# Kernel optimization log

Measured on AMD Instinct MI355X. Metric: run time of the kernel, lower is better.

## Reference

```python
import jax, jax.numpy as jnp
import numpy as np

D_MODEL = 1024
NUM_HEAD = 16
D_HEAD = D_MODEL // NUM_HEAD


def setup_inputs() -> dict:
    key = jax.random.key(0)
    kx, kq, kk, kv, ko = jax.random.split(key, 5)
    x = jax.random.normal(kx, (2, 2048, D_MODEL), dtype=jnp.float32)
    p_q = jax.random.normal(kq, (D_MODEL, D_MODEL), dtype=jnp.float32)
    p_k = jax.random.normal(kk, (D_MODEL, D_MODEL), dtype=jnp.float32)
    p_v = jax.random.normal(kv, (D_MODEL, D_MODEL), dtype=jnp.float32)
    p_o = jax.random.normal(ko, (D_MODEL, D_MODEL), dtype=jnp.float32)
    return {"x": x, "p_q": p_q, "p_k": p_k, "p_v": p_v, "p_o": p_o}


def reference(x, p_q, p_k, p_v, p_o):
    B, S, _ = x.shape
    # project: weight viewed as [H, d_head, d_model]; out[b,h,s,d] = sum_m x[b,s,m] W[h,d,m]
    wq = p_q.reshape(NUM_HEAD, D_HEAD, D_MODEL)
    wk = p_k.reshape(NUM_HEAD, D_HEAD, D_MODEL)
    wv = p_v.reshape(NUM_HEAD, D_HEAD, D_MODEL)
    q = jnp.einsum('bsm,hdm->bhsd', x, wq)
    k = jnp.einsum('bsm,hdm->bhsd', x, wk)
    v = jnp.einsum('bsm,hdm->bhsd', x, wv)
    # full causal attention, scores scaled by 1/sqrt(d_head)
    scores = jnp.einsum('bhqd,bhkd->bhqk', q, k) / jnp.sqrt(jnp.float32(D_HEAD))
    causal = jnp.tril(jnp.ones((S, S), dtype=bool))
    scores = jnp.where(causal, scores, -jnp.inf)
    attn = jax.nn.softmax(scores, axis=-1)
    out = jnp.einsum('bhqk,bhkd->bhqd', attn, v)
    out = out.transpose(0, 2, 1, 3).reshape(B, S, D_MODEL)  # [B,S,H*d_head]
    # output proj: einsum '... d1, d2 d1 -> ... d2' == out @ p_o.T
    return jnp.einsum('bsm,nm->bsn', out, p_o)
```

## Files before the change

### kernel.cpp

```cpp
#include <hip/hip_runtime.h>
#include <stdint.h>

#define D_MODEL 1024
#define SEQ     2048
#define NHEAD   16
#define BATCH   2
#define NROWS   (BATCH*SEQ)

typedef _Float16 f16;
typedef _Float16 f16x8 __attribute__((ext_vector_type(8)));
typedef _Float16 f16x4 __attribute__((ext_vector_type(4)));
typedef __fp16   h16x2 __attribute__((ext_vector_type(2)));
typedef float    f32x4 __attribute__((ext_vector_type(4)));

#define MFMA16 __builtin_amdgcn_mfma_f32_16x16x32_f16

__device__ __forceinline__ void gload16(const void* g, void* l) {
  __builtin_amdgcn_global_load_lds(
      (const __attribute__((address_space(1))) void*)g,
      (__attribute__((address_space(3))) void*)l, 16, 0, 0);
}

__device__ __forceinline__ int pkh2(float a, float b) {
  union { h16x2 h; int i; } u;
  u.h = __builtin_amdgcn_cvt_pkrtz(a, b);
  return u.i;
}

__global__ void split4_kernel(const float* __restrict__ in, f16* __restrict__ hi,
                              f16* __restrict__ lo, int n4, float scale) {
  int i = blockIdx.x * blockDim.x + threadIdx.x;
  if (i >= n4) return;
  float4 v = reinterpret_cast<const float4*>(in)[i];
  v.x *= scale; v.y *= scale; v.z *= scale; v.w *= scale;
  f16x4 h, l4;
  h[0] = (f16)v.x; h[1] = (f16)v.y; h[2] = (f16)v.z; h[3] = (f16)v.w;
  l4[0] = (f16)(v.x - (float)h[0]);
  l4[1] = (f16)(v.y - (float)h[1]);
  l4[2] = (f16)(v.z - (float)h[2]);
  l4[3] = (f16)(v.w - (float)h[3]);
  *reinterpret_cast<f16x4*>(hi + 4*(size_t)i) = h;
  *reinterpret_cast<f16x4*>(lo + 4*(size_t)i) = l4;
}

__global__ void prep_w_kernel(const float* __restrict__ pq, const float* __restrict__ pk,
                              const float* __restrict__ pv, const float* __restrict__ po,
                              f16* __restrict__ wq_hi, f16* __restrict__ wq_lo,
                              f16* __restrict__ wk_hi, f16* __restrict__ wk_lo,
                              f16* __restrict__ wv_h,  f16* __restrict__ wo_h,
                              int n4, float qscale) {
  int i = blockIdx.x * blockDim.x + threadIdx.x;
  if (i >= n4) return;
  {
    float4 v = reinterpret_cast<const float4*>(pq)[i];
    v.x *= qscale; v.y *= qscale; v.z *= qscale; v.w *= qscale;
    f16x4 h, l4;
    h[0] = (f16)v.x; h[1] = (f16)v.y; h[2] = (f16)v.z; h[3] = (f16)v.w;
    l4[0] = (f16)(v.x - (float)h[0]); l4[1] = (f16)(v.y - (float)h[1]);
    l4[2] = (f16)(v.z - (float)h[2]); l4[3] = (f16)(v.w - (float)h[3]);
    *reinterpret_cast<f16x4*>(wq_hi + 4*(size_t)i) = h;
    *reinterpret_cast<f16x4*>(wq_lo + 4*(size_t)i) = l4;
  }
  {
    float4 v = reinterpret_cast<const float4*>(pk)[i];
    f16x4 h, l4;
    h[0] = (f16)v.x; h[1] = (f16)v.y; h[2] = (f16)v.z; h[3] = (f16)v.w;
    l4[0] = (f16)(v.x - (float)h[0]); l4[1] = (f16)(v.y - (float)h[1]);
    l4[2] = (f16)(v.z - (float)h[2]); l4[3] = (f16)(v.w - (float)h[3]);
    *reinterpret_cast<f16x4*>(wk_hi + 4*(size_t)i) = h;
    *reinterpret_cast<f16x4*>(wk_lo + 4*(size_t)i) = l4;
  }
  {
    float4 v = reinterpret_cast<const float4*>(pv)[i];
    f16x4 h;
    h[0] = (f16)v.x; h[1] = (f16)v.y; h[2] = (f16)v.z; h[3] = (f16)v.w;
    *reinterpret_cast<f16x4*>(wv_h + 4*(size_t)i) = h;
  }
  {
    float4 v = reinterpret_cast<const float4*>(po)[i];
    f16x4 h;
    h[0] = (f16)v.x; h[1] = (f16)v.y; h[2] = (f16)v.z; h[3] = (f16)v.w;
    *reinterpret_cast<f16x4*>(wo_h + 4*(size_t)i) = h;
  }
}

template<bool F32_OUT, bool COLCHUNK>
__global__ __launch_bounds__(256, 2)
void gemm_nt(const f16* __restrict__ Ahi,
             const f16* __restrict__ Bhi,
             f16* __restrict__ Chi, float* __restrict__ Cf,
             int M, int N, int K)
{
  constexpr int B_OFF  = 8192;
  constexpr int STRIDE = 12288;
  __shared__ __align__(16) char smem[2 * STRIDE];

  const int tid = threadIdx.x;
  const int w = tid >> 6, l = tid & 63;
  const int wr = (w >> 1) * 64;
  const int wc = (w & 1) * 32;

  const int gx = gridDim.x, gy = gridDim.y;
  const int nwg = gx * gy;
  const int flat = blockIdx.y * gx + blockIdx.x;
  const int swz = (flat & 7) * (nwg >> 3) + (flat >> 3);
  const int bxn = COLCHUNK ? (swz / gy) : (swz % gx);
  const int byn = COLCHUNK ? (swz % gy) : (swz / gx);
  const int bm = byn * 128, bn = bxn * 64;

  f32x4 acc[4][2] = {};

  const int srow = tid >> 2;
  const int schunk = 8 * (((tid & 3) ^ ((srow >> 1) & 3)));

  auto stage = [&](int kt) {
    char* dst = smem + (kt & 1) * STRIDE;
    const int k0 = kt * 32;
    const f16* ga = Ahi + (size_t)(bm + srow) * K + k0 + schunk;
    gload16(ga,        dst + (w << 10));
    gload16(ga + 64*K, dst + 4096 + (w << 10));
    const f16* gb = Bhi + (size_t)(bn + srow) * K + k0 + schunk;
    gload16(gb,        dst + B_OFF + (w << 10));
  };

  const int nkt = K >> 5;
  stage(0);

  for (int kt = 0; kt < nkt; kt++) {
    if (kt + 1 < nkt) {
      stage(kt + 1);
      asm volatile("s_waitcnt vmcnt(3)" ::: "memory");
    } else {
      asm volatile("s_waitcnt vmcnt(0)" ::: "memory");
    }
    __builtin_amdgcn_s_barrier();

    const char* buf = smem + (kt & 1) * STRIDE;
    const int ar = (l & 15);
    const int ak = 16 * ((l >> 4) ^ ((ar >> 1) & 3));
    f16x8 a_hi[4];
#pragma unroll
    for (int mi = 0; mi < 4; mi++)
      a_hi[mi] = *(const f16x8*)(buf + (size_t)(wr + mi*16 + ar) * 64 + ak);
    __builtin_amdgcn_s_setprio(1);
#pragma unroll
    for (int ni = 0; ni < 2; ni++) {
      f16x8 b_hi = *(const f16x8*)(buf + B_OFF + (size_t)(wc + ni*16 + ar) * 64 + ak);
#pragma unroll
      for (int mi = 0; mi < 4; mi++)
        acc[mi][ni] = MFMA16(a_hi[mi], b_hi, acc[mi][ni], 0, 0, 0);
    }
    __builtin_amdgcn_s_setprio(0);
    __builtin_amdgcn_s_barrier();
  }

  const int crow0 = bm + wr + (l >> 4) * 4;
  const int ccol0 = bn + wc + (l & 15);
#pragma unroll
  for (int mi = 0; mi < 4; mi++) {
#pragma unroll
    for (int ni = 0; ni < 2; ni++) {
#pragma unroll
      for (int j = 0; j < 4; j++) {
        size_t idx = (size_t)(crow0 + mi*16 + j) * N + (ccol0 + ni*16);
        float v = acc[mi][ni][j];
        if (F32_OUT) Cf[idx] = v;
        else         Chi[idx] = (f16)v;
      }
    }
  }
}

__global__ __launch_bounds__(256, 2)
void gemm_qk(const f16* __restrict__ Ahi, const f16* __restrict__ Alo,
             const f16* __restrict__ Bqh, const f16* __restrict__ Bql,
             const f16* __restrict__ Bkh, const f16* __restrict__ Bkl,
             f16* __restrict__ Qh, f16* __restrict__ Qlo2,
             f16* __restrict__ Kh, f16* __restrict__ Klo2)
{
  constexpr int N = D_MODEL, K = D_MODEL;
  constexpr int STRIDE = 32768;
  __shared__ __align__(16) char smem[2 * STRIDE];

  const int tid = threadIdx.x;
  const int w = tid >> 6, l = tid & 63;
  const int wr = (w >> 1) * 64;
  const int wc = (w & 1) * 32;

  const int flat = blockIdx.y * 16 + blockIdx.x;
  const int swz = (flat & 7) * 64 + (flat >> 3);
  const int bm = (swz / 16) * 128, bn = (swz % 16) * 64;

  f32x4 accQ[4][2] = {}, accK[4][2] = {};

  const int srow = tid >> 2;
  const int schunk = 8 * (((tid & 3) ^ ((srow >> 1) & 3)));

  auto stage = [&](int kt) {
    char* dst = smem + (kt & 1) * STRIDE;
    const int k0 = kt * 32;
    const f16* ga = Ahi + (size_t)(bm + srow) * K + k0 + schunk;
    gload16(ga,        dst + (w << 10));
    gload16(ga + 64*K, dst + 4096 + (w << 10));
    const f16* gal = Alo + (size_t)(bm + srow) * K + k0 + schunk;
    gload16(gal,        dst + 8192 + (w << 10));
    gload16(gal + 64*K, dst + 12288 + (w << 10));
    const size_t bo = (size_t)(bn + srow) * K + k0 + schunk;
    gload16(Bqh + bo, dst + 16384 + (w << 10));
    gload16(Bql + bo, dst + 20480 + (w << 10));
    gload16(Bkh + bo, dst + 24576 + (w << 10));
    gload16(Bkl + bo, dst + 28672 + (w << 10));
  };

  const int nkt = K >> 5;
  stage(0);

  for (int kt = 0; kt < nkt; kt++) {
    if (kt + 1 < nkt) {
      stage(kt + 1);
      asm volatile("s_waitcnt vmcnt(8)" ::: "memory");
    } else {
      asm volatile("s_waitcnt vmcnt(0)" ::: "memory");
    }
    __builtin_amdgcn_s_barrier();

    const char* buf = smem + (kt & 1) * STRIDE;
    const int ar = (l & 15);
    const int ak = 16 * ((l >> 4) ^ ((ar >> 1) & 3));
    f16x8 a_hi[4], a_lo[4];
#pragma unroll
    for (int mi = 0; mi < 4; mi++) {
      a_hi[mi] = *(const f16x8*)(buf + (size_t)(wr + mi*16 + ar) * 64 + ak);
      a_lo[mi] = *(const f16x8*)(buf + 8192 + (size_t)(wr + mi*16 + ar) * 64 + ak);
    }
    __builtin_amdgcn_s_setprio(1);
#pragma unroll
    for (int ni = 0; ni < 2; ni++) {
      const int bo = (wc + ni*16 + ar) * 64 + ak;
      f16x8 bqh = *(const f16x8*)(buf + 16384 + bo);
      f16x8 bql = *(const f16x8*)(buf + 20480 + bo);
      f16x8 bkh = *(const f16x8*)(buf + 24576 + bo);
      f16x8 bkl = *(const f16x8*)(buf + 28672 + bo);
#pragma unroll
      for (int mi = 0; mi < 4; mi++) {
        accQ[mi][ni] = MFMA16(a_hi[mi], bqh, accQ[mi][ni], 0, 0, 0);
        accQ[mi][ni] = MFMA16(a_hi[mi], bql, accQ[mi][ni], 0, 0, 0);
        accQ[mi][ni] = MFMA16(a_lo[mi], bqh, accQ[mi][ni], 0, 0, 0);
        accK[mi][ni] = MFMA16(a_hi[mi], bkh, accK[mi][ni], 0, 0, 0);
        accK[mi][ni] = MFMA16(a_hi[mi], bkl, accK[mi][ni], 0, 0, 0);
        accK[mi][ni] = MFMA16(a_lo[mi], bkh, accK[mi][ni], 0, 0, 0);
      }
    }
    __builtin_amdgcn_s_setprio(0);
    __builtin_amdgcn_s_barrier();
  }

  const int crow0 = bm + wr + (l >> 4) * 4;
  const int ccol0 = bn + wc + (l & 15);
#pragma unroll
  for (int mi = 0; mi < 4; mi++) {
#pragma unroll
    for (int ni = 0; ni < 2; ni++) {
#pragma unroll
      for (int j = 0; j < 4; j++) {
        size_t idx = (size_t)(crow0 + mi*16 + j) * N + (ccol0 + ni*16);
        float qv = accQ[mi][ni][j];
        f16 qh = (f16)qv;
        Qh[idx] = qh;  Qlo2[idx] = (f16)(qv - (float)qh);
        float kv = accK[mi][ni][j];
        f16 kh = (f16)kv;
        Kh[idx] = kh;  Klo2[idx] = (f16)(kv - (float)kh);
      }
    }
  }
}

__global__ __launch_bounds__(512, 4)
void attn_kernel(const f16* __restrict__ Qhi, const f16* __restrict__ Qlo,
                 const f16* __restrict__ Khi, const f16* __restrict__ Klo,
                 const f16* __restrict__ VT, f16* __restrict__ Out)
{
  __shared__ __align__(16) char smem[49152];

  const int tid = threadIdx.x, w = tid >> 6, l = tid & 63;
  const int g = l >> 4, q4 = l & 15;
  const int wi = w & 3, grp = w >> 2;
  const int flat = blockIdx.x;
  const int xcd = flat & 7, slot = flat >> 3;
  const int bh = xcd * 4 + (slot >> 4);
  const int c = slot & 15;
  const int b = bh >> 4, h = bh & 15;
  const int bS = b * SEQ;
  const size_t hoff = (size_t)h * 64;
  const int T  = 64 - 2 * c;
  const int P1 = 2 * c + 2;
  const int P2 = 31 - 2 * c;

  int qw = (grp ? (31 - c) : c) * 64 + wi * 16;

  f16x8 qh[2], ql[2];
  auto loadQ = [&]() {
#pragma unroll
    for (int ks = 0; ks < 2; ks++) {
      const size_t base = (size_t)(bS + qw + q4) * D_MODEL + hoff + ks * 32 + g * 8;
      qh[ks] = *(const f16x8*)(Qhi + base);
      ql[ks] = *(const f16x8*)(Qlo + base);
    }
  };
  loadQ();

  f32x4 o[4] = {};
  float m_run = -INFINITY, l_run = 0.f;

  const int k_src = 8 * ((l & 7) ^ (l >> 3));
  const int v_src = 8 * ((l & 3) ^ ((l >> 2) & 3));

  auto stage = [&](int t) {
    const int kv0 = t * 32;
    char* sb = smem + (t & 3) * 12288;
    if (w < 4) {
      const f16* src = (w < 2) ? Khi : Klo;
      char* dstc = sb + ((w < 2) ? 0 : 4096);
      const int wi2 = w & 1;
#pragma unroll
      for (int gi = 0; gi < 2; gi++) {
        const int sub = 2 * wi2 + gi;
        const int row = 8 * sub + (l >> 3);
        gload16(src + (size_t)(bS + kv0 + row) * D_MODEL + hoff + k_src,
                dstc + sub * 1024);
      }
    } else if (w < 6) {
      const int wi2 = w - 4;
#pragma unroll
      for (int gi = 0; gi < 2; gi++) {
        const int sub = 2 * wi2 + gi;
        const int drow = 16 * sub + (l >> 2);
        gload16(VT + (hoff + drow) * (size_t)NROWS + bS + kv0 + v_src,
                sb + 8192 + sub * 1024);
      }
    }
  };

  const int idx_lo = (q4 + 32 * (g & 1)) * 4;
  const int idx_hi = idx_lo + 64;
  const bool upper = (l >= 32);

  auto compute = [&](int t) {
    const char* sb = smem + (t & 3) * 12288;
    const int kv0 = t * 32;

    f32x4 s[2] = {};
    __builtin_amdgcn_s_setprio(1);
#pragma unroll
    for (int ni = 0; ni < 2; ni++) {
      const int row = ni * 16 + q4;
#pragma unroll
      for (int ks = 0; ks < 2; ks++) {
        const int boff = row * 128 + 16 * ((ks * 4 + g) ^ (row & 7));
        f16x8 kh8 = *(const f16x8*)(sb + boff);
        f16x8 kl8 = *(const f16x8*)(sb + 4096 + boff);
        s[ni] = MFMA16(kh8, qh[ks], s[ni], 0, 0, 0);
        s[ni] = MFMA16(kh8, ql[ks], s[ni], 0, 0, 0);
        s[ni] = MFMA16(kl8, qh[ks], s[ni], 0, 0, 0);
      }
    }
    __builtin_amdgcn_s_setprio(0);

    const bool need_mask = (kv0 + 31) > qw;
    const int q_abs = qw + q4;
    float p[2][4];
    float pm = -INFINITY;
#pragma unroll
    for (int ni = 0; ni < 2; ni++)
#pragma unroll
      for (int j = 0; j < 4; j++) {
        float v = s[ni][j];
        if (need_mask && (kv0 + ni * 16 + 4 * g + j) > q_abs) v = -INFINITY;
        p[ni][j] = v;
        pm = fmaxf(pm, v);
      }
    pm = fmaxf(pm, __shfl_xor(pm, 16));
    pm = fmaxf(pm, __shfl_xor(pm, 32));

    if (!__all(pm - m_run <= 8.0f)) {
      const float mn = fmaxf(m_run, pm);
      const float sc = __builtin_amdgcn_exp2f(m_run - mn);
      m_run = mn;
      l_run *= sc;
#pragma unroll
      for (int nd = 0; nd < 4; nd++)
#pragma unroll
        for (int j = 0; j < 4; j++) o[nd][j] *= sc;
    }
    float ps = 0.f;
#pragma unroll
    for (int ni = 0; ni < 2; ni++)
#pragma unroll
      for (int j = 0; j < 4; j++) {
        const float e = __builtin_amdgcn_exp2f(p[ni][j] - m_run);
        p[ni][j] = e;
        ps += e;
      }
    ps += __shfl_xor(ps, 16);
    ps += __shfl_xor(ps, 32);
    l_run += ps;

    const int pk0 = pkh2(p[0][0], p[0][1]);
    const int pk1 = pkh2(p[0][2], p[0][3]);
    const int pk2 = pkh2(p[1][0], p[1][1]);
    const int pk3 = pkh2(p[1][2], p[1][3]);
    const int b0l = __builtin_amdgcn_ds_bpermute(idx_lo, pk0);
    const int b2l = __builtin_amdgcn_ds_bpermute(idx_lo, pk2);
    const int b1l = __builtin_amdgcn_ds_bpermute(idx_lo, pk1);
    const int b3l = __builtin_amdgcn_ds_bpermute(idx_lo, pk3);
    const int b0h = __builtin_amdgcn_ds_bpermute(idx_hi, pk0);
    const int b2h = __builtin_amdgcn_ds_bpermute(idx_hi, pk2);
    const int b1h = __builtin_amdgcn_ds_bpermute(idx_hi, pk1);
    const int b3h = __builtin_amdgcn_ds_bpermute(idx_hi, pk3);
    union { int u[4]; f16x8 v; } pu;
    pu.u[0] = upper ? b2l : b0l;
    pu.u[1] = upper ? b3l : b1l;
    pu.u[2] = upper ? b2h : b0h;
    pu.u[3] = upper ? b3h : b1h;
    const f16x8 pa = pu.v;

    __builtin_amdgcn_s_setprio(1);
#pragma unroll
    for (int nd = 0; nd < 4; nd++) {
      const int d = nd * 16 + q4;
      f16x8 bv = *(const f16x8*)(sb + 8192 + d * 64 + 16 * (g ^ (d & 3)));
      o[nd] = MFMA16(bv, pa, o[nd], 0, 0, 0);
    }
    __builtin_amdgcn_s_setprio(0);
  };

  stage(0);
  stage(1);

  for (int t = 0; t < P1; t++) {
    stage(t + 2);
    asm volatile("s_waitcnt vmcnt(4)" ::: "memory");
    __builtin_amdgcn_s_barrier();
    compute(t);
    __builtin_amdgcn_s_barrier();
  }

  if (grp == 0) {
    const float inv = 1.0f / l_run;
    const size_t rowb = (size_t)(bS + qw + q4) * D_MODEL + hoff;
#pragma unroll
    for (int nd = 0; nd < 4; nd++) {
      f16x4 v;
#pragma unroll
      for (int j = 0; j < 4; j++) v[j] = (f16)(o[nd][j] * inv);
      *reinterpret_cast<f16x4*>(Out + rowb + nd * 16 + 4 * g) = v;
    }
    qw = (31 - c) * 64 + wi * 16;
    loadQ();
#pragma unroll
    for (int nd = 0; nd < 4; nd++)
#pragma unroll
      for (int j = 0; j < 4; j++) o[nd][j] = 0.f;
    m_run = -INFINITY;
    l_run = 0.f;
  }

  for (int j = 0; j < P2; j++) {
    const int u = P1 + 2 * j;
    const bool st = (u + 3) < T;
    if (st) { stage(u + 2); stage(u + 3); }
    if (st) asm volatile("s_waitcnt vmcnt(4)" ::: "memory");
    else    asm volatile("s_waitcnt vmcnt(0)" ::: "memory");
    __builtin_amdgcn_s_barrier();
    compute(u + grp);
    __builtin_amdgcn_s_barrier();
  }

  if (grp == 0) {
    float* mb = (float*)smem + wi * 1152 + l * 18;
#pragma unroll
    for (int nd = 0; nd < 4; nd++)
#pragma unroll
      for (int j = 0; j < 4; j++) mb[nd * 4 + j] = o[nd][j];
    mb[16] = m_run;
    mb[17] = l_run;
  }
  __syncthreads();
  if (grp == 1) {
    const float* mb = (const float*)smem + wi * 1152 + l * 18;
    const float m2 = mb[16], l2 = mb[17];
    const float mm = fmaxf(m_run, m2);
    const float a1 = __builtin_amdgcn_exp2f(m_run - mm);
    const float a2 = __builtin_amdgcn_exp2f(m2 - mm);
    const float inv = 1.0f / (l_run * a1 + l2 * a2);
    const size_t rowb = (size_t)(bS + qw + q4) * D_MODEL + hoff;
#pragma unroll
    for (int nd = 0; nd < 4; nd++) {
      f16x4 v;
#pragma unroll
      for (int j = 0; j < 4; j++)
        v[j] = (f16)((o[nd][j] * a1 + mb[nd * 4 + j] * a2) * inv);
      *reinterpret_cast<f16x4*>(Out + rowb + nd * 16 + 4 * g) = v;
    }
  }
}

extern "C" void kernel_launch(void* const* d_in, const int* in_sizes, int n_in,
                              void* d_out, int out_size, void* d_ws, size_t ws_size,
                              hipStream_t stream) {
  const float* x  = (const float*)d_in[0];
  const float* pq = (const float*)d_in[1];
  const float* pk = (const float*)d_in[2];
  const float* pv = (const float*)d_in[3];
  const float* po = (const float*)d_in[4];
  float* out = (float*)d_out;

  char* ws = (char*)d_ws;
  size_t off = 0;
  auto alloc = [&](size_t elems) {
    f16* p = (f16*)(ws + off);
    off += ((elems * 2 + 255) & ~(size_t)255);
    return p;
  };
  f16* x_hi  = alloc((size_t)NROWS * D_MODEL);
  f16* x_lo  = alloc((size_t)NROWS * D_MODEL);
  f16* wq_hi = alloc((size_t)D_MODEL * D_MODEL);
  f16* wq_lo = alloc((size_t)D_MODEL * D_MODEL);
  f16* wk_hi = alloc((size_t)D_MODEL * D_MODEL);
  f16* wk_lo = alloc((size_t)D_MODEL * D_MODEL);
  f16* wv_h  = alloc((size_t)D_MODEL * D_MODEL);
  f16* wo_h  = alloc((size_t)D_MODEL * D_MODEL);
  f16* q_hi  = alloc((size_t)NROWS * D_MODEL);
  f16* q_lo  = alloc((size_t)NROWS * D_MODEL);
  f16* k_hi  = alloc((size_t)NROWS * D_MODEL);
  f16* k_lo  = alloc((size_t)NROWS * D_MODEL);
  f16* vt    = alloc((size_t)NROWS * D_MODEL);
  f16* ao    = alloc((size_t)NROWS * D_MODEL);

  const int n4x = NROWS * D_MODEL / 4;
  const int n4w = D_MODEL * D_MODEL / 4;
  const float qscale = 0.125f * 1.44269504088896f;
  split4_kernel<<<n4x/256, 256, 0, stream>>>(x, x_hi, x_lo, n4x, 1.0f);
  prep_w_kernel<<<n4w/256, 256, 0, stream>>>(pq, pk, pv, po,
                                             wq_hi, wq_lo, wk_hi, wk_lo, wv_h, wo_h,
                                             n4w, qscale);

  gemm_qk<<<dim3(16, 32), 256, 0, stream>>>(x_hi, x_lo, wq_hi, wq_lo, wk_hi, wk_lo,
                                            q_hi, q_lo, k_hi, k_lo);
  dim3 gv(NROWS/64, D_MODEL/128);
  gemm_nt<false, true><<<gv, 256, 0, stream>>>(wv_h, x_hi, vt, nullptr, D_MODEL, NROWS, D_MODEL);

  attn_kernel<<<dim3(512), 512, 0, stream>>>(q_hi, q_lo, k_hi, k_lo, vt, ao);

  dim3 gg(D_MODEL/64, NROWS/128);
  gemm_nt<true, false><<<gg, 256, 0, stream>>>(ao, wo_h, nullptr, out, NROWS, D_MODEL, D_MODEL);
}
```

Measured before the change: 166.2 us.

## Enlarge GEMM tiles and triple-buffer QK projection with interleaved prefetch

gemm_nt moves from 128x64 to 128x128 output tiles per workgroup, with each wave computing a 64x64 block and a unified staging loop, to raise data reuse per loaded tile. gemm_qk becomes a 512-thread, 256x64-tile kernel with a three-stage LDS ring buffer, where prefetches two tiles ahead are spread across four compute phases separated by barriers. The goal is to hide global load latency and cut redundant operand fetches. The cost is much more shared memory (144KB for gemm_qk), more barriers per iteration, and fewer workgroups in the grid.

New measurement: 256.5 us. 54.3% more time.

```diff
diff --git a/kernel.cpp b/kernel.cpp
--- a/kernel.cpp
+++ b/kernel.cpp
@@ -85,20 +85,18 @@
 }
 
 template<bool F32_OUT, bool COLCHUNK>
-__global__ __launch_bounds__(256, 2)
-void gemm_nt(const f16* __restrict__ Ahi,
-             const f16* __restrict__ Bhi,
-             f16* __restrict__ Chi, float* __restrict__ Cf,
+__global__ __launch_bounds__(256, 4)
+void gemm_nt(const f16* __restrict__ A, const f16* __restrict__ B,
+             f16* __restrict__ Ch, float* __restrict__ Cf,
              int M, int N, int K)
 {
-  constexpr int B_OFF  = 8192;
-  constexpr int STRIDE = 12288;
+  constexpr int STRIDE = 16384;
   __shared__ __align__(16) char smem[2 * STRIDE];
 
   const int tid = threadIdx.x;
   const int w = tid >> 6, l = tid & 63;
   const int wr = (w >> 1) * 64;
-  const int wc = (w & 1) * 32;
+  const int wc = (w & 1) * 64;
 
   const int gx = gridDim.x, gy = gridDim.y;
   const int nwg = gx * gy;
@@ -106,21 +104,24 @@
   const int swz = (flat & 7) * (nwg >> 3) + (flat >> 3);
   const int bxn = COLCHUNK ? (swz / gy) : (swz % gx);
   const int byn = COLCHUNK ? (swz % gy) : (swz / gx);
-  const int bm = byn * 128, bn = bxn * 64;
-
-  f32x4 acc[4][2] = {};
-
-  const int srow = tid >> 2;
-  const int schunk = 8 * (((tid & 3) ^ ((srow >> 1) & 3)));
+  const int bm = byn * 128, bn = bxn * 128;
+
+  f32x4 acc[4][4] = {};
+
+  const int rl = l >> 2;
+  const int sc = 8 * ((l & 3) ^ ((l >> 3) & 3));
 
   auto stage = [&](int kt) {
     char* dst = smem + (kt & 1) * STRIDE;
     const int k0 = kt * 32;
-    const f16* ga = Ahi + (size_t)(bm + srow) * K + k0 + schunk;
-    gload16(ga,        dst + (w << 10));
-    gload16(ga + 64*K, dst + 4096 + (w << 10));
-    const f16* gb = Bhi + (size_t)(bn + srow) * K + k0 + schunk;
-    gload16(gb,        dst + B_OFF + (w << 10));
+#pragma unroll
+    for (int i = 0; i < 4; i++) {
+      const int s = i * 4 + w;
+      const f16* base = (s < 8) ? A : B;
+      const int row0 = (s < 8) ? (bm + s * 16) : (bn + (s - 8) * 16);
+      gload16(base + (size_t)(row0 + rl) * K + k0 + sc,
+              dst + ((s < 8) ? 0 : 8192) + (s & 7) * 1024);
+    }
   };
 
   const int nkt = K >> 5;
@@ -129,27 +130,28 @@
   for (int kt = 0; kt < nkt; kt++) {
     if (kt + 1 < nkt) {
       stage(kt + 1);
-      asm volatile("s_waitcnt vmcnt(3)" ::: "memory");
+      asm volatile("s_waitcnt vmcnt(4)" ::: "memory");
     } else {
       asm volatile("s_waitcnt vmcnt(0)" ::: "memory");
     }
     __builtin_amdgcn_s_barrier();
 
     const char* buf = smem + (kt & 1) * STRIDE;
-    const int ar = (l & 15);
+    const int ar = l & 15;
     const int ak = 16 * ((l >> 4) ^ ((ar >> 1) & 3));
-    f16x8 a_hi[4];
+    f16x8 a[4], b[4];
 #pragma unroll
     for (int mi = 0; mi < 4; mi++)
-      a_hi[mi] = *(const f16x8*)(buf + (size_t)(wr + mi*16 + ar) * 64 + ak);
+      a[mi] = *(const f16x8*)(buf + (size_t)(wr + mi*16 + ar) * 64 + ak);
+#pragma unroll
+    for (int ni = 0; ni < 4; ni++)
+      b[ni] = *(const f16x8*)(buf + 8192 + (size_t)(wc + ni*16 + ar) * 64 + ak);
     __builtin_amdgcn_s_setprio(1);
 #pragma unroll
-    for (int ni = 0; ni < 2; ni++) {
-      f16x8 b_hi = *(const f16x8*)(buf + B_OFF + (size_t)(wc + ni*16 + ar) * 64 + ak);
+    for (int ni = 0; ni < 4; ni++)
 #pragma unroll
       for (int mi = 0; mi < 4; mi++)
-        acc[mi][ni] = MFMA16(a_hi[mi], b_hi, acc[mi][ni], 0, 0, 0);
-    }
+        acc[mi][ni] = MFMA16(a[mi], b[ni], acc[mi][ni], 0, 0, 0);
     __builtin_amdgcn_s_setprio(0);
     __builtin_amdgcn_s_barrier();
   }
@@ -159,99 +161,142 @@
 #pragma unroll
   for (int mi = 0; mi < 4; mi++) {
 #pragma unroll
-    for (int ni = 0; ni < 2; ni++) {
+    for (int ni = 0; ni < 4; ni++) {
 #pragma unroll
       for (int j = 0; j < 4; j++) {
         size_t idx = (size_t)(crow0 + mi*16 + j) * N + (ccol0 + ni*16);
         float v = acc[mi][ni][j];
         if (F32_OUT) Cf[idx] = v;
-        else         Chi[idx] = (f16)v;
+        else         Ch[idx] = (f16)v;
       }
     }
   }
 }
 
-__global__ __launch_bounds__(256, 2)
+__global__ __launch_bounds__(512, 2)
 void gemm_qk(const f16* __restrict__ Ahi, const f16* __restrict__ Alo,
              const f16* __restrict__ Bqh, const f16* __restrict__ Bql,
              const f16* __restrict__ Bkh, const f16* __restrict__ Bkl,
              f16* __restrict__ Qh, f16* __restrict__ Qlo2,
              f16* __restrict__ Kh, f16* __restrict__ Klo2)
 {
-  constexpr int N = D_MODEL, K = D_MODEL;
-  constexpr int STRIDE = 32768;
-  __shared__ __align__(16) char smem[2 * STRIDE];
+  constexpr int K = D_MODEL, N = D_MODEL;
+  constexpr int BUF = 49152;
+  constexpr int KT = 32;
+  __shared__ __align__(16) char smem[3 * BUF];
 
   const int tid = threadIdx.x;
   const int w = tid >> 6, l = tid & 63;
-  const int wr = (w >> 1) * 64;
-  const int wc = (w & 1) * 32;
+  const int wr = (w & 3) * 64;
+  const int wc = (w >> 2) * 32;
 
   const int flat = blockIdx.y * 16 + blockIdx.x;
-  const int swz = (flat & 7) * 64 + (flat >> 3);
-  const int bm = (swz / 16) * 128, bn = (swz % 16) * 64;
+  const int swz = (flat & 7) * 32 + (flat >> 3);
+  const int bm = (swz >> 4) * 256, bn = (swz & 15) * 64;
 
   f32x4 accQ[4][2] = {}, accK[4][2] = {};
 
-  const int srow = tid >> 2;
-  const int schunk = 8 * (((tid & 3) ^ ((srow >> 1) & 3)));
-
-  auto stage = [&](int kt) {
-    char* dst = smem + (kt & 1) * STRIDE;
-    const int k0 = kt * 32;
-    const f16* ga = Ahi + (size_t)(bm + srow) * K + k0 + schunk;
-    gload16(ga,        dst + (w << 10));
-    gload16(ga + 64*K, dst + 4096 + (w << 10));
-    const f16* gal = Alo + (size_t)(bm + srow) * K + k0 + schunk;
-    gload16(gal,        dst + 8192 + (w << 10));
-    gload16(gal + 64*K, dst + 12288 + (w << 10));
-    const size_t bo = (size_t)(bn + srow) * K + k0 + schunk;
-    gload16(Bqh + bo, dst + 16384 + (w << 10));
-    gload16(Bql + bo, dst + 20480 + (w << 10));
-    gload16(Bkh + bo, dst + 24576 + (w << 10));
-    gload16(Bkl + bo, dst + 28672 + (w << 10));
+  const int rl = l >> 2;
+  const int sc = 8 * ((l & 3) ^ ((l >> 3) & 3));
+
+  auto stage2 = [&](int t, int i) {
+    char* buf = smem + (t % 3) * BUF;
+    const int k0 = t * 32;
+    const int s = i * 8 + w;
+    if (s < 32) {
+      const f16* base = (s < 16) ? Ahi : Alo;
+      const int row0 = bm + ((s & 15) << 4);
+      gload16(base + (size_t)(row0 + rl) * K + k0 + sc,
+              buf + ((s < 16) ? 0 : 16384) + ((s & 15) << 10));
+    } else {
+      const int arr = (s - 32) >> 2;
+      const f16* base = arr == 0 ? Bqh : arr == 1 ? Bql : arr == 2 ? Bkh : Bkl;
+      const int row0 = bn + ((s & 3) << 4);
+      gload16(base + (size_t)(row0 + rl) * K + k0 + sc,
+              buf + 32768 + arr * 4096 + ((s & 3) << 10));
+    }
   };
 
-  const int nkt = K >> 5;
-  stage(0);
-
-  for (int kt = 0; kt < nkt; kt++) {
-    if (kt + 1 < nkt) {
-      stage(kt + 1);
-      asm volatile("s_waitcnt vmcnt(8)" ::: "memory");
-    } else {
-      asm volatile("s_waitcnt vmcnt(0)" ::: "memory");
-    }
-    __builtin_amdgcn_s_barrier();
-
-    const char* buf = smem + (kt & 1) * STRIDE;
-    const int ar = (l & 15);
+#pragma unroll
+  for (int i = 0; i < 6; i++) stage2(0, i);
+#pragma unroll
+  for (int i = 0; i < 6; i++) stage2(1, i);
+  asm volatile("s_waitcnt vmcnt(6)" ::: "memory");
+  __builtin_amdgcn_s_barrier();
+
+  for (int t = 0; t < KT; t++) {
+    const char* buf = smem + (t % 3) * BUF;
+    const bool pf = (t + 2 < KT);
+    const int ar = l & 15;
     const int ak = 16 * ((l >> 4) ^ ((ar >> 1) & 3));
-    f16x8 a_hi[4], a_lo[4];
+    const int bo0 = (wc + ar) * 64 + ak;
+    const int bo1 = (wc + 16 + ar) * 64 + ak;
+    f16x8 a_hi[4], a_lo[4], b0, b1;
+
 #pragma unroll
     for (int mi = 0; mi < 4; mi++) {
       a_hi[mi] = *(const f16x8*)(buf + (size_t)(wr + mi*16 + ar) * 64 + ak);
-      a_lo[mi] = *(const f16x8*)(buf + 8192 + (size_t)(wr + mi*16 + ar) * 64 + ak);
-    }
+      a_lo[mi] = *(const f16x8*)(buf + 16384 + (size_t)(wr + mi*16 + ar) * 64 + ak);
+    }
+    b0 = *(const f16x8*)(buf + 32768 + bo0);
+    b1 = *(const f16x8*)(buf + 36864 + bo0);
+    if (pf) { stage2(t + 2, 0); stage2(t + 2, 1); }
+    __builtin_amdgcn_s_barrier();
+    asm volatile("s_waitcnt lgkmcnt(0)" ::: "memory");
     __builtin_amdgcn_s_setprio(1);
 #pragma unroll
-    for (int ni = 0; ni < 2; ni++) {
-      const int bo = (wc + ni*16 + ar) * 64 + ak;
-      f16x8 bqh = *(const f16x8*)(buf + 16384 + bo);
-      f16x8 bql = *(const f16x8*)(buf + 20480 + bo);
-      f16x8 bkh = *(const f16x8*)(buf + 24576 + bo);
-      f16x8 bkl = *(const f16x8*)(buf + 28672 + bo);
-#pragma unroll
-      for (int mi = 0; mi < 4; mi++) {
-        accQ[mi][ni] = MFMA16(a_hi[mi], bqh, accQ[mi][ni], 0, 0, 0);
-        accQ[mi][ni] = MFMA16(a_hi[mi], bql, accQ[mi][ni], 0, 0, 0);
-        accQ[mi][ni] = MFMA16(a_lo[mi], bqh, accQ[mi][ni], 0, 0, 0);
-        accK[mi][ni] = MFMA16(a_hi[mi], bkh, accK[mi][ni], 0, 0, 0);
-        accK[mi][ni] = MFMA16(a_hi[mi], bkl, accK[mi][ni], 0, 0, 0);
-        accK[mi][ni] = MFMA16(a_lo[mi], bkh, accK[mi][ni], 0, 0, 0);
-      }
+    for (int mi = 0; mi < 4; mi++) {
+      accQ[mi][0] = MFMA16(a_hi[mi], b0, accQ[mi][0], 0, 0, 0);
+      accQ[mi][0] = MFMA16(a_hi[mi], b1, accQ[mi][0], 0, 0, 0);
+      accQ[mi][0] = MFMA16(a_lo[mi], b0, accQ[mi][0], 0, 0, 0);
     }
     __builtin_amdgcn_s_setprio(0);
+    __builtin_amdgcn_s_barrier();
+
+    b0 = *(const f16x8*)(buf + 40960 + bo0);
+    b1 = *(const f16x8*)(buf + 45056 + bo0);
+    if (pf) { stage2(t + 2, 2); stage2(t + 2, 3); }
+    __builtin_amdgcn_s_barrier();
+    asm volatile("s_waitcnt lgkmcnt(0)" ::: "memory");
+    __builtin_amdgcn_s_setprio(1);
+#pragma unroll
+    for (int mi = 0; mi < 4; mi++) {
+      accK[mi][0] = MFMA16(a_hi[mi], b0, accK[mi][0], 0, 0, 0);
+      accK[mi][0] = MFMA16(a_hi[mi], b1, accK[mi][0], 0, 0, 0);
+      accK[mi][0] = MFMA16(a_lo[mi], b0, accK[mi][0], 0, 0, 0);
+    }
+    __builtin_amdgcn_s_setprio(0);
+    __builtin_amdgcn_s_barrier();
+
+    b0 = *(const f16x8*)(buf + 32768 + bo1);
+    b1 = *(const f16x8*)(buf + 36864 + bo1);
+    if (pf) { stage2(t + 2, 4); stage2(t + 2, 5); }
+    __builtin_amdgcn_s_barrier();
+    asm volatile("s_waitcnt lgkmcnt(0)" ::: "memory");
+    __builtin_amdgcn_s_setprio(1);
+#pragma unroll
+    for (int mi = 0; mi < 4; mi++) {
+      accQ[mi][1] = MFMA16(a_hi[mi], b0, accQ[mi][1], 0, 0, 0);
+      accQ[mi][1] = MFMA16(a_hi[mi], b1, accQ[mi][1], 0, 0, 0);
+      accQ[mi][1] = MFMA16(a_lo[mi], b0, accQ[mi][1], 0, 0, 0);
+    }
+    __builtin_amdgcn_s_setprio(0);
+    __builtin_amdgcn_s_barrier();
+
+    b0 = *(const f16x8*)(buf + 40960 + bo1);
+    b1 = *(const f16x8*)(buf + 45056 + bo1);
+    __builtin_amdgcn_s_barrier();
+    asm volatile("s_waitcnt lgkmcnt(0)" ::: "memory");
+    __builtin_amdgcn_s_setprio(1);
+#pragma unroll
+    for (int mi = 0; mi < 4; mi++) {
+      accK[mi][1] = MFMA16(a_hi[mi], b0, accK[mi][1], 0, 0, 0);
+      accK[mi][1] = MFMA16(a_hi[mi], b1, accK[mi][1], 0, 0, 0);
+      accK[mi][1] = MFMA16(a_lo[mi], b0, accK[mi][1], 0, 0, 0);
+    }
+    __builtin_amdgcn_s_setprio(0);
+    if (pf) asm volatile("s_waitcnt vmcnt(6)" ::: "memory");
+    else    asm volatile("s_waitcnt vmcnt(0)" ::: "memory");
     __builtin_amdgcn_s_barrier();
   }
 
@@ -384,13 +429,13 @@
 
     if (!__all(pm - m_run <= 8.0f)) {
       const float mn = fmaxf(m_run, pm);
-      const float sc = __builtin_amdgcn_exp2f(m_run - mn);
+      const float sc2 = __builtin_amdgcn_exp2f(m_run - mn);
       m_run = mn;
-      l_run *= sc;
+      l_run *= sc2;
 #pragma unroll
       for (int nd = 0; nd < 4; nd++)
 #pragma unroll
-        for (int j = 0; j < 4; j++) o[nd][j] *= sc;
+        for (int j = 0; j < 4; j++) o[nd][j] *= sc2;
     }
     float ps = 0.f;
 #pragma unroll
@@ -545,13 +590,13 @@
                                              wq_hi, wq_lo, wk_hi, wk_lo, wv_h, wo_h,
                                              n4w, qscale);
 
-  gemm_qk<<<dim3(16, 32), 256, 0, stream>>>(x_hi, x_lo, wq_hi, wq_lo, wk_hi, wk_lo,
+  gemm_qk<<<dim3(16, 16), 512, 0, stream>>>(x_hi, x_lo, wq_hi, wq_lo, wk_hi, wk_lo,
                                             q_hi, q_lo, k_hi, k_lo);
-  dim3 gv(NROWS/64, D_MODEL/128);
+  dim3 gv(NROWS/128, D_MODEL/128);
   gemm_nt<false, true><<<gv, 256, 0, stream>>>(wv_h, x_hi, vt, nullptr, D_MODEL, NROWS, D_MODEL);
 
   attn_kernel<<<dim3(512), 512, 0, stream>>>(q_hi, q_lo, k_hi, k_lo, vt, ao);
 
-  dim3 gg(D_MODEL/64, NROWS/128);
+  dim3 gg(D_MODEL/128, NROWS/128);
   gemm_nt<true, false><<<gg, 256, 0, stream>>>(ao, wo_h, nullptr, out, NROWS, D_MODEL, D_MODEL);
 }
```

## Widen gemm_nt tiles to 128x128 and skip fully-masked causal KV tiles in attention

Applied to the files above, without the earlier changes.

The NT GEMM used for the V and output projections now computes a 128x128 tile per workgroup instead of 128x64. Each wave holds 4x4 accumulators, and the A and B tiles are staged with four async loads per thread. This raises data reuse per LDS load and halves the grid size. In attention, warps skip compute for KV tiles lying entirely above their causal diagonal, which removes wasted MFMA and softmax work. The costs are higher register pressure despite the tighter launch-bounds hint, and fewer workgroups to fill the GPU.

Result: slower. 170.0 us (+2.3%).

```diff
diff --git a/kernel.cpp b/kernel.cpp
--- a/kernel.cpp
+++ b/kernel.cpp
@@ -85,20 +85,18 @@
 }
 
 template<bool F32_OUT, bool COLCHUNK>
-__global__ __launch_bounds__(256, 2)
-void gemm_nt(const f16* __restrict__ Ahi,
-             const f16* __restrict__ Bhi,
-             f16* __restrict__ Chi, float* __restrict__ Cf,
+__global__ __launch_bounds__(256, 4)
+void gemm_nt(const f16* __restrict__ A, const f16* __restrict__ B,
+             f16* __restrict__ Ch, float* __restrict__ Cf,
              int M, int N, int K)
 {
-  constexpr int B_OFF  = 8192;
-  constexpr int STRIDE = 12288;
+  constexpr int STRIDE = 16384;
   __shared__ __align__(16) char smem[2 * STRIDE];
 
   const int tid = threadIdx.x;
   const int w = tid >> 6, l = tid & 63;
   const int wr = (w >> 1) * 64;
-  const int wc = (w & 1) * 32;
+  const int wc = (w & 1) * 64;
 
   const int gx = gridDim.x, gy = gridDim.y;
   const int nwg = gx * gy;
@@ -106,21 +104,24 @@
   const int swz = (flat & 7) * (nwg >> 3) + (flat >> 3);
   const int bxn = COLCHUNK ? (swz / gy) : (swz % gx);
   const int byn = COLCHUNK ? (swz % gy) : (swz / gx);
-  const int bm = byn * 128, bn = bxn * 64;
-
-  f32x4 acc[4][2] = {};
-
-  const int srow = tid >> 2;
-  const int schunk = 8 * (((tid & 3) ^ ((srow >> 1) & 3)));
+  const int bm = byn * 128, bn = bxn * 128;
+
+  f32x4 acc[4][4] = {};
+
+  const int rl = l >> 2;
+  const int sc = 8 * ((l & 3) ^ ((l >> 3) & 3));
 
   auto stage = [&](int kt) {
     char* dst = smem + (kt & 1) * STRIDE;
     const int k0 = kt * 32;
-    const f16* ga = Ahi + (size_t)(bm + srow) * K + k0 + schunk;
-    gload16(ga,        dst + (w << 10));
-    gload16(ga + 64*K, dst + 4096 + (w << 10));
-    const f16* gb = Bhi + (size_t)(bn + srow) * K + k0 + schunk;
-    gload16(gb,        dst + B_OFF + (w << 10));
+#pragma unroll
+    for (int i = 0; i < 4; i++) {
+      const int s = i * 4 + w;
+      const f16* base = (s < 8) ? A : B;
+      const int row0 = (s < 8) ? (bm + s * 16) : (bn + (s - 8) * 16);
+      gload16(base + (size_t)(row0 + rl) * K + k0 + sc,
+              dst + ((s < 8) ? 0 : 8192) + (s & 7) * 1024);
+    }
   };
 
   const int nkt = K >> 5;
@@ -129,27 +130,28 @@
   for (int kt = 0; kt < nkt; kt++) {
     if (kt + 1 < nkt) {
       stage(kt + 1);
-      asm volatile("s_waitcnt vmcnt(3)" ::: "memory");
+      asm volatile("s_waitcnt vmcnt(4)" ::: "memory");
     } else {
       asm volatile("s_waitcnt vmcnt(0)" ::: "memory");
     }
     __builtin_amdgcn_s_barrier();
 
     const char* buf = smem + (kt & 1) * STRIDE;
-    const int ar = (l & 15);
+    const int ar = l & 15;
     const int ak = 16 * ((l >> 4) ^ ((ar >> 1) & 3));
-    f16x8 a_hi[4];
+    f16x8 a[4], b[4];
 #pragma unroll
     for (int mi = 0; mi < 4; mi++)
-      a_hi[mi] = *(const f16x8*)(buf + (size_t)(wr + mi*16 + ar) * 64 + ak);
+      a[mi] = *(const f16x8*)(buf + (size_t)(wr + mi*16 + ar) * 64 + ak);
+#pragma unroll
+    for (int ni = 0; ni < 4; ni++)
+      b[ni] = *(const f16x8*)(buf + 8192 + (size_t)(wc + ni*16 + ar) * 64 + ak);
     __builtin_amdgcn_s_setprio(1);
 #pragma unroll
-    for (int ni = 0; ni < 2; ni++) {
-      f16x8 b_hi = *(const f16x8*)(buf + B_OFF + (size_t)(wc + ni*16 + ar) * 64 + ak);
+    for (int ni = 0; ni < 4; ni++)
 #pragma unroll
       for (int mi = 0; mi < 4; mi++)
-        acc[mi][ni] = MFMA16(a_hi[mi], b_hi, acc[mi][ni], 0, 0, 0);
-    }
+        acc[mi][ni] = MFMA16(a[mi], b[ni], acc[mi][ni], 0, 0, 0);
     __builtin_amdgcn_s_setprio(0);
     __builtin_amdgcn_s_barrier();
   }
@@ -159,13 +161,13 @@
 #pragma unroll
   for (int mi = 0; mi < 4; mi++) {
 #pragma unroll
-    for (int ni = 0; ni < 2; ni++) {
+    for (int ni = 0; ni < 4; ni++) {
 #pragma unroll
       for (int j = 0; j < 4; j++) {
         size_t idx = (size_t)(crow0 + mi*16 + j) * N + (ccol0 + ni*16);
         float v = acc[mi][ni][j];
         if (F32_OUT) Cf[idx] = v;
-        else         Chi[idx] = (f16)v;
+        else         Ch[idx] = (f16)v;
       }
     }
   }
@@ -384,13 +386,13 @@
 
     if (!__all(pm - m_run <= 8.0f)) {
       const float mn = fmaxf(m_run, pm);
-      const float sc = __builtin_amdgcn_exp2f(m_run - mn);
+      const float sc2 = __builtin_amdgcn_exp2f(m_run - mn);
       m_run = mn;
-      l_run *= sc;
+      l_run *= sc2;
 #pragma unroll
       for (int nd = 0; nd < 4; nd++)
 #pragma unroll
-        for (int j = 0; j < 4; j++) o[nd][j] *= sc;
+        for (int j = 0; j < 4; j++) o[nd][j] *= sc2;
     }
     float ps = 0.f;
 #pragma unroll
@@ -441,7 +443,7 @@
     stage(t + 2);
     asm volatile("s_waitcnt vmcnt(4)" ::: "memory");
     __builtin_amdgcn_s_barrier();
-    compute(t);
+    if (32 * t <= qw + 15) compute(t);
     __builtin_amdgcn_s_barrier();
   }
 
@@ -547,11 +549,11 @@
 
   gemm_qk<<<dim3(16, 32), 256, 0, stream>>>(x_hi, x_lo, wq_hi, wq_lo, wk_hi, wk_lo,
                                             q_hi, q_lo, k_hi, k_lo);
-  dim3 gv(NROWS/64, D_MODEL/128);
+  dim3 gv(NROWS/128, D_MODEL/128);
   gemm_nt<false, true><<<gv, 256, 0, stream>>>(wv_h, x_hi, vt, nullptr, D_MODEL, NROWS, D_MODEL);
 
   attn_kernel<<<dim3(512), 512, 0, stream>>>(q_hi, q_lo, k_hi, k_lo, vt, ao);
 
-  dim3 gg(D_MODEL/64, NROWS/128);
+  dim3 gg(D_MODEL/128, NROWS/128);
   gemm_nt<true, false><<<gg, 256, 0, stream>>>(ao, wo_h, nullptr, out, NROWS, D_MODEL, D_MODEL);
 }
```

## Use 64-wide KV tiles with double buffering in first attention phase

Applied to the files above, without the earlier changes.

The first phase of the causal attention loop now processes 64 keys per iteration instead of 32, staging K hi/lo and V^T into two 24KB buffers with all 8 waves loading. This halves the number of barriers and softmax-rescale passes in that phase and lets more MFMAs issue per synchronization. The cost is higher register pressure from the larger score and probability arrays, plus the switch from 4-deep to 2-deep prefetch. The second phase keeps 32-wide tiles and is now primed explicitly after the first loop.

After: 166.1 us. No clear change (-0.1%).

```diff
diff --git a/kernel.cpp b/kernel.cpp
--- a/kernel.cpp
+++ b/kernel.cpp
@@ -314,8 +314,119 @@
 
   const int k_src = 8 * ((l & 7) ^ (l >> 3));
   const int v_src = 8 * ((l & 3) ^ ((l >> 2) & 3));
-
-  auto stage = [&](int t) {
+  const int rowloc = w * 8 + (l >> 3);
+
+  const int idx_lo = (q4 + 32 * (g & 1)) * 4;
+  const int idx_hi = idx_lo + 64;
+  const bool upper = (l >= 32);
+
+  auto stage64 = [&](int t) {
+    const int kv0 = t * 64;
+    char* dst = smem + (t & 1) * 24576;
+    const size_t krow = (size_t)(bS + kv0 + rowloc) * D_MODEL + hoff + k_src;
+    gload16(Khi + krow, dst + (w << 10));
+    gload16(Klo + krow, dst + 8192 + (w << 10));
+    const size_t vrow = (hoff + rowloc) * (size_t)NROWS + bS + kv0 + k_src;
+    gload16(VT + vrow, dst + 16384 + (w << 10));
+  };
+
+  auto compute64 = [&](int t) {
+    const char* buf = smem + (t & 1) * 24576;
+    const int kv0 = t * 64;
+
+    f32x4 s[4] = {};
+    __builtin_amdgcn_s_setprio(1);
+#pragma unroll
+    for (int ni = 0; ni < 4; ni++) {
+      const int row = ni * 16 + q4;
+#pragma unroll
+      for (int ks = 0; ks < 2; ks++) {
+        const int boff = row * 128 + 16 * ((ks * 4 + g) ^ (row & 7));
+        f16x8 kh8 = *(const f16x8*)(buf + boff);
+        f16x8 kl8 = *(const f16x8*)(buf + 8192 + boff);
+        s[ni] = MFMA16(kh8, qh[ks], s[ni], 0, 0, 0);
+        s[ni] = MFMA16(kh8, ql[ks], s[ni], 0, 0, 0);
+        s[ni] = MFMA16(kl8, qh[ks], s[ni], 0, 0, 0);
+      }
+    }
+    __builtin_amdgcn_s_setprio(0);
+
+    const bool need_mask = (kv0 + 63) > qw;
+    const int q_abs = qw + q4;
+    float p[4][4];
+    float pm = -INFINITY;
+#pragma unroll
+    for (int ni = 0; ni < 4; ni++)
+#pragma unroll
+      for (int j = 0; j < 4; j++) {
+        float v = s[ni][j];
+        if (need_mask && (kv0 + ni * 16 + 4 * g + j) > q_abs) v = -INFINITY;
+        p[ni][j] = v;
+        pm = fmaxf(pm, v);
+      }
+    pm = fmaxf(pm, __shfl_xor(pm, 16));
+    pm = fmaxf(pm, __shfl_xor(pm, 32));
+
+    if (!__all(pm - m_run <= 8.0f)) {
+      const float mn = fmaxf(m_run, pm);
+      const float sc2 = __builtin_amdgcn_exp2f(m_run - mn);
+      m_run = mn;
+      l_run *= sc2;
+#pragma unroll
+      for (int nd = 0; nd < 4; nd++)
+#pragma unroll
+        for (int j = 0; j < 4; j++) o[nd][j] *= sc2;
+    }
+    float ps = 0.f;
+#pragma unroll
+    for (int ni = 0; ni < 4; ni++)
+#pragma unroll
+      for (int j = 0; j < 4; j++) {
+        const float e = __builtin_amdgcn_exp2f(p[ni][j] - m_run);
+        p[ni][j] = e;
+        ps += e;
+      }
+    ps += __shfl_xor(ps, 16);
+    ps += __shfl_xor(ps, 32);
+    l_run += ps;
+
+    f16x8 pa[2];
+#pragma unroll
+    for (int h2 = 0; h2 < 2; h2++) {
+      const int pk0 = pkh2(p[2*h2][0],   p[2*h2][1]);
+      const int pk1 = pkh2(p[2*h2][2],   p[2*h2][3]);
+      const int pk2 = pkh2(p[2*h2+1][0], p[2*h2+1][1]);
+      const int pk3 = pkh2(p[2*h2+1][2], p[2*h2+1][3]);
+      const int b0l = __builtin_amdgcn_ds_bpermute(idx_lo, pk0);
+      const int b2l = __builtin_amdgcn_ds_bpermute(idx_lo, pk2);
+      const int b1l = __builtin_amdgcn_ds_bpermute(idx_lo, pk1);
+      const int b3l = __builtin_amdgcn_ds_bpermute(idx_lo, pk3);
+      const int b0h = __builtin_amdgcn_ds_bpermute(idx_hi, pk0);
+      const int b2h = __builtin_amdgcn_ds_bpermute(idx_hi, pk2);
+      const int b1h = __builtin_amdgcn_ds_bpermute(idx_hi, pk1);
+      const int b3h = __builtin_amdgcn_ds_bpermute(idx_hi, pk3);
+      union { int u[4]; f16x8 v; } pu;
+      pu.u[0] = upper ? b2l : b0l;
+      pu.u[1] = upper ? b3l : b1l;
+      pu.u[2] = upper ? b2h : b0h;
+      pu.u[3] = upper ? b3h : b1h;
+      pa[h2] = pu.v;
+    }
+
+    __builtin_amdgcn_s_setprio(1);
+#pragma unroll
+    for (int nd = 0; nd < 4; nd++) {
+      const int d = nd * 16 + q4;
+#pragma unroll
+      for (int h2 = 0; h2 < 2; h2++) {
+        f16x8 bv = *(const f16x8*)(buf + 16384 + d * 128 + 16 * ((h2 * 4 + g) ^ (d & 7)));
+        o[nd] = MFMA16(bv, pa[h2], o[nd], 0, 0, 0);
+      }
+    }
+    __builtin_amdgcn_s_setprio(0);
+  };
+
+  auto stage32 = [&](int t) {
     const int kv0 = t * 32;
     char* sb = smem + (t & 3) * 12288;
     if (w < 4) {
@@ -341,11 +452,7 @@
     }
   };
 
-  const int idx_lo = (q4 + 32 * (g & 1)) * 4;
-  const int idx_hi = idx_lo + 64;
-  const bool upper = (l >= 32);
-
-  auto compute = [&](int t) {
+  auto compute32 = [&](int t) {
     const char* sb = smem + (t & 3) * 12288;
     const int kv0 = t * 32;
 
@@ -384,13 +491,13 @@
 
     if (!__all(pm - m_run <= 8.0f)) {
       const float mn = fmaxf(m_run, pm);
-      const float sc = __builtin_amdgcn_exp2f(m_run - mn);
+      const float sc2 = __builtin_amdgcn_exp2f(m_run - mn);
       m_run = mn;
-      l_run *= sc;
+      l_run *= sc2;
 #pragma unroll
       for (int nd = 0; nd < 4; nd++)
 #pragma unroll
-        for (int j = 0; j < 4; j++) o[nd][j] *= sc;
+        for (int j = 0; j < 4; j++) o[nd][j] *= sc2;
     }
     float ps = 0.f;
 #pragma unroll
@@ -434,14 +541,16 @@
     __builtin_amdgcn_s_setprio(0);
   };
 
-  stage(0);
-  stage(1);
-
-  for (int t = 0; t < P1; t++) {
-    stage(t + 2);
-    asm volatile("s_waitcnt vmcnt(4)" ::: "memory");
-    __builtin_amdgcn_s_barrier();
-    compute(t);
+  stage64(0);
+  for (int t = 0; t <= c; t++) {
+    if (t + 1 <= c) {
+      stage64(t + 1);
+      asm volatile("s_waitcnt vmcnt(3)" ::: "memory");
+    } else {
+      asm volatile("s_waitcnt vmcnt(0)" ::: "memory");
+    }
+    __builtin_amdgcn_s_barrier();
+    compute64(t);
     __builtin_amdgcn_s_barrier();
   }
 
@@ -465,14 +574,16 @@
     l_run = 0.f;
   }
 
+  stage32(P1);
+  stage32(P1 + 1);
   for (int j = 0; j < P2; j++) {
     const int u = P1 + 2 * j;
     const bool st = (u + 3) < T;
-    if (st) { stage(u + 2); stage(u + 3); }
+    if (st) { stage32(u + 2); stage32(u + 3); }
     if (st) asm volatile("s_waitcnt vmcnt(4)" ::: "memory");
     else    asm volatile("s_waitcnt vmcnt(0)" ::: "memory");
     __builtin_amdgcn_s_barrier();
-    compute(u + grp);
+    compute32(u + grp);
     __builtin_amdgcn_s_barrier();
   }
 
```
